# Optimization experiments

Measured on AMD Instinct MI355X. Metric: run time of the kernel, lower is better.

The kernel has to match this reference:

```python
import jax, jax.numpy as jnp
import numpy as np

B, N, I, H = 1024, 16, 256, 1024
V = 0.08  # init_var


def setup_inputs() -> dict:
    key = jax.random.key(0)
    ks = jax.random.split(key, 16)
    inp = jax.random.normal(ks[0], (B, N, I), jnp.float32)
    p = (jax.random.uniform(ks[1], (B, N, N)) > 0.3).astype(jnp.float32)
    phis = jnp.maximum(p, jnp.eye(N, dtype=jnp.float32)[None])  # ensure >=1 valid slot per row
    u = lambda k, s: jax.random.uniform(k, s, jnp.float32, -V, V)
    return {
        'input': inp, 'phis': phis,
        'init_token': jnp.zeros((I,), jnp.float32),
        'W1': u(ks[2], (H, H)), 'W2': u(ks[3], (H, H)), 'v': u(ks[4], (H, 1)),
        'Wih_e': u(ks[5], (3 * H, I)), 'Whh_e': u(ks[6], (3 * H, H)),
        'bih_e': u(ks[7], (3 * H,)), 'bhh_e': u(ks[8], (3 * H,)),
        'Wih_d': u(ks[9], (3 * H, I)), 'Whh_d': u(ks[10], (3 * H, H)),
        'bih_d': u(ks[11], (3 * H,)), 'bhh_d': u(ks[12], (3 * H,)),
    }


def gru_cell(x, h, Wih, Whh, bih, bhh):
    # torch.nn.GRUCell semantics; gate order [r, z, n]
    gi = x @ Wih.T + bih
    gh = h @ Whh.T + bhh
    ir, iz, ig = jnp.split(gi, 3, -1)
    hr, hz, hg = jnp.split(gh, 3, -1)
    r = jax.nn.sigmoid(ir + hr)
    z = jax.nn.sigmoid(iz + hz)
    g = jnp.tanh(ig + r * hg)
    return (1 - z) * g + z * h


def masked_softmax(mask, u):
    # faithful to softmax_m: mask before max, mask exps, normalize
    um = u * mask
    m = jnp.max(um, 1, keepdims=True)
    e = jnp.exp(um - m) * mask
    return e / jnp.sum(e, 1, keepdims=True)


def reference(input, phis, init_token, W1, W2, v,
              Wih_e, Whh_e, bih_e, bhh_e, Wih_d, Whh_d, bih_d, bhh_d):
    # gating scalar t_n = phis[:, n, n-1]; t_0 := 1 (no-op at step 0)
    t_gate = jnp.concatenate(
        [jnp.ones((B, 1), input.dtype), jnp.diagonal(phis, -1, 1, 2)], axis=1).T  # (N, B)

    # ---- Encoder ----
    def enc_step(h, xs):
        x, t = xs
        h = gru_cell(x, t[:, None] * h, Wih_e, Whh_e, bih_e, bhh_e)
        return h, h

    _, henc = jax.lax.scan(enc_step, jnp.zeros((B, H), input.dtype),
                           (input.transpose(1, 0, 2), t_gate))
    hidden_encoder = henc.transpose(1, 0, 2)  # (B, N, H)

    # ---- Decoder ----
    Ns = phis.sum(2)                                             # (B, N)
    idx_seq = ((Ns + jnp.arange(N)[None] - 1) % N).astype(jnp.int32)  # (B, N)
    bidx = jnp.arange(B)
    hidden0 = hidden_encoder[bidx, ((Ns[:, 0] - 1) % N).astype(jnp.int32)]  # (B, H)
    W1xe = jnp.einsum('bnh,hk->bnk', hidden_encoder, W1)         # (B, N, H)
    start = jnp.broadcast_to(init_token, (B, I))

    def dec_step(carry, xs):
        hidden, inp_step = carry
        t, idx, mask = xs
        init_h = hidden_encoder[bidx, idx]
        hidden = t[:, None] * hidden + (1 - t)[:, None] * init_h
        inp_step = t[:, None] * inp_step + (1 - t)[:, None] * start
        hidden = gru_cell(inp_step, hidden, Wih_d, Whh_d, bih_d, bhh_d)
        u = jnp.squeeze(jnp.tanh(W1xe + (hidden @ W2)[:, None, :]) @ v, -1)  # (B, N)
        attn = masked_softmax(mask, u)
        inp_step = jnp.einsum('bn,bni->bi', attn, input)
        return (hidden, inp_step), attn

    _, attns = jax.lax.scan(dec_step, (hidden0, start),
                            (t_gate, idx_seq.T, phis.transpose(1, 0, 2)))
    return attns.transpose(1, 0, 2)  # (B, N, N)
```

## Files before the change

kernel.cpp:

```cpp
#include <hip/hip_runtime.h>
#include <math.h>

#define B_  1024
#define N_  16
#define I_  256
#define H_  1024
#define H3_ 3072

typedef _Float16 f16;
typedef _Float16 f16x4 __attribute__((ext_vector_type(4)));
typedef _Float16 f16x8 __attribute__((ext_vector_type(8)));
typedef float    f32x4 __attribute__((ext_vector_type(4)));

__device__ __forceinline__ float sigmoidf_(float x) { return 1.f / (1.f + expf(-x)); }

__device__ __forceinline__ void lds_write_row(f16* dst, int row, int s, f16x8 vv)
{
    int key = (row >> 1) & 3;
    int g0  = (((s & 1) * 2 + 0) ^ key);
    int g1  = (((s & 1) * 2 + 1) ^ key);
    f16x4 lo = {vv[0], vv[1], vv[2], vv[3]};
    f16x4 hi = {vv[4], vv[5], vv[6], vv[7]};
    *(f16x4*)((char*)dst + row * 64 + g0 * 16 + (s >> 1) * 8) = lo;
    *(f16x4*)((char*)dst + row * 64 + g1 * 16 + (s >> 1) * 8) = hi;
}

__global__ void precompute_kernel(const float* __restrict__ phis,
                                  float* __restrict__ tg,
                                  int* __restrict__ idx)
{
    int b = blockIdx.x * blockDim.x + threadIdx.x;
    if (b >= B_) return;
    tg[b] = 1.0f;
    for (int t = 1; t < N_; ++t)
        tg[t * B_ + b] = phis[(size_t)b * N_ * N_ + t * N_ + (t - 1)];
    tg[16 * B_ + b] = 0.0f;
    for (int t = 0; t < N_; ++t) {
        float ns = 0.f;
        for (int k = 0; k < N_; ++k) ns += phis[(size_t)b * N_ * N_ + t * N_ + k];
        int nsi = (int)(ns + 0.5f);
        idx[b * N_ + t] = (nsi + t - 1) % N_;
    }
}

__global__ void cast_kernel(const float* __restrict__ in, f16* __restrict__ out, int n)
{
    int i = blockIdx.x * blockDim.x + threadIdx.x;
    if (i < n) out[i] = (f16)in[i];
}

__global__ void cast4_kernel(const float* __restrict__ s0, f16* __restrict__ d0, int n0,
                             const float* __restrict__ s1, f16* __restrict__ d1, int n1,
                             const float* __restrict__ s2, f16* __restrict__ d2, int n2,
                             const float* __restrict__ s3, f16* __restrict__ d3, int n3)
{
    int i = blockIdx.x * blockDim.x + threadIdx.x;
    int T0 = n0, T1 = T0 + n1, T2 = T1 + n2, T3 = T2 + n3;
    if (i < T0) d0[i] = (f16)s0[i];
    else if (i < T1) d1[i - T0] = (f16)s1[i - T0];
    else if (i < T2) d2[i - T1] = (f16)s2[i - T1];
    else if (i < T3) d3[i - T2] = (f16)s3[i - T2];
}

__global__ __launch_bounds__(256) void transpose_cast2_kernel(
    const float* __restrict__ in0, f16* __restrict__ out0,
    const float* __restrict__ in1, f16* __restrict__ out1)
{
    const float* in  = blockIdx.z ? in1 : in0;
    f16*        outp = blockIdx.z ? out1 : out0;
    __shared__ float tile[32][33];
    int bx = blockIdx.x * 32, by = blockIdx.y * 32;
    int tx = threadIdx.x & 31, ty = threadIdx.x >> 5;
#pragma unroll
    for (int r = 0; r < 32; r += 8)
        tile[ty + r][tx] = in[(size_t)(by + ty + r) * H_ + bx + tx];
    __syncthreads();
#pragma unroll
    for (int r = 0; r < 32; r += 8)
        outp[(size_t)(bx + ty + r) * H_ + by + tx] = (f16)tile[tx][ty + r];
}

template <typename OutT>
__global__ __launch_bounds__(256) void hgemm_kernel(
    const f16* __restrict__ A, int lda,
    const f16* __restrict__ Bt, int ldb,
    OutT* __restrict__ C, int ldc, int K)
{
    __shared__ char smem[32768];

    const int tid  = threadIdx.x;
    const int lane = tid & 63;
    const int wid  = tid >> 6;
    const int wr   = wid >> 1;
    const int wc   = wid & 1;
    const int rsel = lane & 15;
    const int kb   = lane >> 4;

    int flat = blockIdx.y * gridDim.x + blockIdx.x;
    int nwg  = gridDim.x * gridDim.y;
    int cpx  = nwg >> 3;
    int nf   = (flat & 7) * cpx + (flat >> 3);
    const int n0 = (int)(nf % gridDim.x) * 128;
    const int m0 = (int)(nf / gridDim.x) * 128;

    const int strow0 = tid >> 2;
    const int strow1 = 64 + (tid >> 2);
    const int sts    = tid & 3;

    f32x4 acc[4][4];
#pragma unroll
    for (int m = 0; m < 4; ++m)
#pragma unroll
        for (int n = 0; n < 4; ++n) acc[m][n] = (f32x4)0.f;

    f16x8 sA0, sA1, sB0, sB1;
    f16x8 tA0, tA1, tB0, tB1;
    auto GL0 = [&](int k0) {
        sA0 = *(const f16x8*)(A + (size_t)(m0 + strow0) * lda + k0 + sts * 8);
        sA1 = *(const f16x8*)(A + (size_t)(m0 + strow1) * lda + k0 + sts * 8);
        sB0 = *(const f16x8*)(Bt + (size_t)(n0 + strow0) * ldb + k0 + sts * 8);
        sB1 = *(const f16x8*)(Bt + (size_t)(n0 + strow1) * ldb + k0 + sts * 8);
    };
    auto GL1 = [&](int k0) {
        tA0 = *(const f16x8*)(A + (size_t)(m0 + strow0) * lda + k0 + sts * 8);
        tA1 = *(const f16x8*)(A + (size_t)(m0 + strow1) * lda + k0 + sts * 8);
        tB0 = *(const f16x8*)(Bt + (size_t)(n0 + strow0) * ldb + k0 + sts * 8);
        tB1 = *(const f16x8*)(Bt + (size_t)(n0 + strow1) * ldb + k0 + sts * 8);
    };
    auto LW0 = [&](int c) {
        f16* As_ = (f16*)(smem + c * 8192);
        f16* Bs_ = (f16*)(smem + 16384 + c * 8192);
        lds_write_row(As_, strow0, sts, sA0);
        lds_write_row(As_, strow1, sts, sA1);
        lds_write_row(Bs_, strow0, sts, sB0);
        lds_write_row(Bs_, strow1, sts, sB1);
    };
    auto LW1 = [&](int c) {
        f16* As_ = (f16*)(smem + c * 8192);
        f16* Bs_ = (f16*)(smem + 16384 + c * 8192);
        lds_write_row(As_, strow0, sts, tA0);
        lds_write_row(As_, strow1, sts, tA1);
        lds_write_row(Bs_, strow0, sts, tB0);
        lds_write_row(Bs_, strow1, sts, tB1);
    };
    auto COMP = [&](int c) {
        char* As_ = smem + c * 8192;
        char* Bs_ = smem + 16384 + c * 8192;
        f16x8 af[4], bf[4];
#pragma unroll
        for (int m = 0; m < 4; ++m) {
            int row = wr * 64 + m * 16 + rsel;
            af[m] = *(const f16x8*)(As_ + row * 64 + ((kb ^ ((row >> 1) & 3)) << 4));
        }
#pragma unroll
        for (int n = 0; n < 4; ++n) {
            int row = wc * 64 + n * 16 + rsel;
            bf[n] = *(const f16x8*)(Bs_ + row * 64 + ((kb ^ ((row >> 1) & 3)) << 4));
        }
#pragma unroll
        for (int m = 0; m < 4; ++m)
#pragma unroll
            for (int n = 0; n < 4; ++n)
                acc[m][n] = __builtin_amdgcn_mfma_f32_16x16x32_f16(af[m], bf[n], acc[m][n], 0, 0, 0);
    };

    const int nk = K / 32;
    GL0(0);
    GL1(32);
    LW0(0);
    __syncthreads();

    for (int ks = 0; ks < nk; ks += 2) {
        if (ks + 2 < nk) GL0((ks + 2) * 32);
        COMP(0);
        LW1(1);
        __syncthreads();
        if (ks + 3 < nk) GL1((ks + 3) * 32);
        COMP(1);
        if (ks + 2 < nk) LW0(0);
        __syncthreads();
    }

#pragma unroll
    for (int m = 0; m < 4; ++m) {
        int row0 = m0 + wr * 64 + m * 16 + kb * 4;
#pragma unroll
        for (int n = 0; n < 4; ++n) {
            int col = n0 + wc * 64 + n * 16 + rsel;
#pragma unroll
            for (int r = 0; r < 4; ++r)
                C[(size_t)(row0 + r) * ldc + col] = (OutT)acc[m][n][r];
        }
    }
}

template <int MODE>
__global__ __launch_bounds__(512) void gru_fused_kernel(
    const f16* __restrict__ A1, int lda1,
    const f16* __restrict__ Bt1, int ldb1, int K1,
    const f16* __restrict__ A2,
    const f16* __restrict__ Bt2,
    const float* __restrict__ bih, const float* __restrict__ bhh,
    float* __restrict__ h,
    const float* __restrict__ tg_cur,
    const float* __restrict__ tg_next,
    f16* __restrict__ out_a,
    f16* __restrict__ hs)
{
    __shared__ char smem[57344];

    const int tid  = threadIdx.x;
    const int wg   = tid >> 8;
    const int ltid = tid & 255;
    const int lane = tid & 63;
    const int wid4 = (ltid >> 6);
    const int wr   = wid4 >> 1;
    const int wc   = wid4 & 1;
    const int rsel = lane & 15;
    const int kb   = lane >> 4;

    char* base = smem + wg * 28672;

    int flat = blockIdx.y * gridDim.x + blockIdx.x;
    int nf   = (flat & 7) * 64 + (flat >> 3);
    const int j0 = (nf >> 5) * 64;
    const int b0 = (nf & 31) * 32;

    const int strow = ltid >> 2;
    const int sts   = ltid & 3;

    f32x4 acc1[3][2], acc2[3][2];
#pragma unroll
    for (int g = 0; g < 3; ++g)
#pragma unroll
        for (int nt = 0; nt < 2; ++nt) { acc1[g][nt] = (f32x4)0.f; acc2[g][nt] = (f32x4)0.f; }

    f16x8 sA, sB0, sB1, sB2;
    f16x8 tA, tB0, tB1, tB2;
    const f16* Ap;  const f16* Btp;  int ldap, ldbp;
    auto GL0 = [&](int k0) {
        if (ltid < 128) sA = *(const f16x8*)(Ap + (size_t)(b0 + strow) * ldap + k0 + sts * 8);
        sB0 = *(const f16x8*)(Btp + (size_t)(0 * H_ + j0 + strow) * ldbp + k0 + sts * 8);
        sB1 = *(const f16x8*)(Btp + (size_t)(1 * H_ + j0 + strow) * ldbp + k0 + sts * 8);
        sB2 = *(const f16x8*)(Btp + (size_t)(2 * H_ + j0 + strow) * ldbp + k0 + sts * 8);
    };
    auto GL1 = [&](int k0) {
        if (ltid < 128) tA = *(const f16x8*)(Ap + (size_t)(b0 + strow) * ldap + k0 + sts * 8);
        tB0 = *(const f16x8*)(Btp + (size_t)(0 * H_ + j0 + strow) * ldbp + k0 + sts * 8);
        tB1 = *(const f16x8*)(Btp + (size_t)(1 * H_ + j0 + strow) * ldbp + k0 + sts * 8);
        tB2 = *(const f16x8*)(Btp + (size_t)(2 * H_ + j0 + strow) * ldbp + k0 + sts * 8);
    };
    auto LW0 = [&](int c) {
        if (ltid < 128) lds_write_row((f16*)(base + c * 2048), strow, sts, sA);
        f16* Bs_ = (f16*)(base + 4096 + c * 12288);
        lds_write_row(Bs_ + 0 * 64 * 32, strow, sts, sB0);
        lds_write_row(Bs_ + 1 * 64 * 32, strow, sts, sB1);
        lds_write_row(Bs_ + 2 * 64 * 32, strow, sts, sB2);
    };
    auto LW1 = [&](int c) {
        if (ltid < 128) lds_write_row((f16*)(base + c * 2048), strow, sts, tA);
        f16* Bs_ = (f16*)(base + 4096 + c * 12288);
        lds_write_row(Bs_ + 0 * 64 * 32, strow, sts, tB0);
        lds_write_row(Bs_ + 1 * 64 * 32, strow, sts, tB1);
        lds_write_row(Bs_ + 2 * 64 * 32, strow, sts, tB2);
    };
    auto COMP = [&](int c, int phase) {
        char* As_ = base + c * 2048;
        char* Bs_ = base + 4096 + c * 12288;
        int arow = wr * 16 + rsel;
        f16x8 af = *(const f16x8*)(As_ + arow * 64 + ((kb ^ ((arow >> 1) & 3)) << 4));
#pragma unroll
        for (int gg = 0; gg < 3; ++gg)
#pragma unroll
            for (int nt = 0; nt < 2; ++nt) {
                int brow = wc * 32 + nt * 16 + rsel;
                f16x8 bf = *(const f16x8*)(Bs_ + (gg * 64 + brow) * 64 +
                                           ((kb ^ ((brow >> 1) & 3)) << 4));
                if (phase == 0)
                    acc1[gg][nt] = __builtin_amdgcn_mfma_f32_16x16x32_f16(af, bf, acc1[gg][nt], 0, 0, 0);
                else
                    acc2[gg][nt] = __builtin_amdgcn_mfma_f32_16x16x32_f16(af, bf, acc2[gg][nt], 0, 0, 0);
            }
    };

#pragma unroll
    for (int phase = 0; phase < 2; ++phase) {
        Ap   = phase ? A2 : A1;
        Btp  = phase ? Bt2 : Bt1;
        ldap = phase ? H_ : lda1;
        ldbp = phase ? H_ : ldb1;
        const int Kp   = phase ? H_ : K1;
        const int half = Kp >> 1;
        const int kbeg = wg * half;
        const int nk   = half >> 5;

        GL0(kbeg);
        GL1(kbeg + 32);
        LW0(0);
        __syncthreads();

        for (int ks = 0; ks < nk; ks += 2) {
            if (ks + 2 < nk) GL0(kbeg + (ks + 2) * 32);
            COMP(0, phase);
            LW1(1);
            __syncthreads();
            if (ks + 3 < nk) GL1(kbeg + (ks + 3) * 32);
            COMP(1, phase);
            if (ks + 2 < nk) LW0(0);
            __syncthreads();
        }
    }

    f32x4* red = (f32x4*)smem;
    if (wg) {
#pragma unroll
        for (int g = 0; g < 3; ++g)
#pragma unroll
            for (int nt = 0; nt < 2; ++nt) red[ltid * 6 + g * 2 + nt] = acc1[g][nt];
    }
    __syncthreads();
    if (!wg) {
#pragma unroll
        for (int g = 0; g < 3; ++g)
#pragma unroll
            for (int nt = 0; nt < 2; ++nt) acc1[g][nt] += red[ltid * 6 + g * 2 + nt];
    }
    __syncthreads();
    if (wg) {
#pragma unroll
        for (int g = 0; g < 3; ++g)
#pragma unroll
            for (int nt = 0; nt < 2; ++nt) red[ltid * 6 + g * 2 + nt] = acc2[g][nt];
    }
    __syncthreads();

    if (!wg) {
#pragma unroll
        for (int g = 0; g < 3; ++g)
#pragma unroll
            for (int nt = 0; nt < 2; ++nt) acc2[g][nt] += red[ltid * 6 + g * 2 + nt];

#pragma unroll
        for (int nt = 0; nt < 2; ++nt) {
            int j = j0 + wc * 32 + nt * 16 + rsel;
            float br_i = bih[j],          br_h = bhh[j];
            float bz_i = bih[H_ + j],     bz_h = bhh[H_ + j];
            float bg_i = bih[2 * H_ + j], bg_h = bhh[2 * H_ + j];
#pragma unroll
            for (int q = 0; q < 4; ++q) {
                int row = b0 + wr * 16 + kb * 4 + q;
                float r = sigmoidf_(acc1[0][nt][q] + br_i + acc2[0][nt][q] + br_h);
                float z = sigmoidf_(acc1[1][nt][q] + bz_i + acc2[1][nt][q] + bz_h);
                float g = tanhf(acc1[2][nt][q] + bg_i + r * (acc2[2][nt][q] + bg_h));
                float leak;
                if (MODE == 0) leak = tg_cur[row] * h[(size_t)row * H_ + j];
                else           leak = h[(size_t)row * H_ + j];
                float hn = (1.f - z) * g + z * leak;
                h[(size_t)row * H_ + j] = hn;
                if (MODE == 0) {
                    out_a[(size_t)row * (N_ * H_) + j] = (f16)hn;
                    hs[(size_t)row * H_ + j] = (f16)(tg_next[row] * hn);
                } else {
                    out_a[(size_t)row * H_ + j] = (f16)hn;
                }
            }
        }
    }
}

__global__ __launch_bounds__(512) void hgemm64_kernel(
    const f16* __restrict__ A, const f16* __restrict__ Bt, float* __restrict__ C)
{
    __shared__ char smem[32768];

    const int tid  = threadIdx.x;
    const int wg   = tid >> 8;
    const int ltid = tid & 255;
    const int lane = tid & 63;
    const int wid4 = (ltid >> 6);
    const int wr   = wid4 >> 1;
    const int wc   = wid4 & 1;
    const int rsel = lane & 15;
    const int kb   = lane >> 4;

    char* base = smem + wg * 16384;

    int flat = blockIdx.y * gridDim.x + blockIdx.x;
    int nf   = (flat & 7) * 32 + (flat >> 3);
    const int m0 = (nf >> 4) * 64;
    const int n0 = (nf & 15) * 64;

    const int strow = ltid >> 2;
    const int sts   = ltid & 3;

    f32x4 acc[2][2];
#pragma unroll
    for (int m = 0; m < 2; ++m)
#pragma unroll
        for (int n = 0; n < 2; ++n) acc[m][n] = (f32x4)0.f;

    f16x8 sA, sB, tA, tB;
    auto GL0 = [&](int k0) {
        sA = *(const f16x8*)(A + (size_t)(m0 + strow) * H_ + k0 + sts * 8);
        sB = *(const f16x8*)(Bt + (size_t)(n0 + strow) * H_ + k0 + sts * 8);
    };
    auto GL1 = [&](int k0) {
        tA = *(const f16x8*)(A + (size_t)(m0 + strow) * H_ + k0 + sts * 8);
        tB = *(const f16x8*)(Bt + (size_t)(n0 + strow) * H_ + k0 + sts * 8);
    };
    auto LW0 = [&](int c) {
        lds_write_row((f16*)(base + c * 4096), strow, sts, sA);
        lds_write_row((f16*)(base + 8192 + c * 4096), strow, sts, sB);
    };
    auto LW1 = [&](int c) {
        lds_write_row((f16*)(base + c * 4096), strow, sts, tA);
        lds_write_row((f16*)(base + 8192 + c * 4096), strow, sts, tB);
    };
    auto COMP = [&](int c) {
        char* As_ = base + c * 4096;
        char* Bs_ = base + 8192 + c * 4096;
        f16x8 af[2], bf[2];
#pragma unroll
        for (int m = 0; m < 2; ++m) {
            int row = wr * 32 + m * 16 + rsel;
            af[m] = *(const f16x8*)(As_ + row * 64 + ((kb ^ ((row >> 1) & 3)) << 4));
        }
#pragma unroll
        for (int nt = 0; nt < 2; ++nt) {
            int row = wc * 32 + nt * 16 + rsel;
            bf[nt] = *(const f16x8*)(Bs_ + row * 64 + ((kb ^ ((row >> 1) & 3)) << 4));
        }
#pragma unroll
        for (int m = 0; m < 2; ++m)
#pragma unroll
            for (int nt = 0; nt < 2; ++nt)
                acc[m][nt] = __builtin_amdgcn_mfma_f32_16x16x32_f16(af[m], bf[nt], acc[m][nt], 0, 0, 0);
    };

    const int kbeg = wg * 512;
    GL0(kbeg);
    GL1(kbeg + 32);
    LW0(0);
    __syncthreads();

    for (int ks = 0; ks < 16; ks += 2) {
        if (ks + 2 < 16) GL0(kbeg + (ks + 2) * 32);
        COMP(0);
        LW1(1);
        __syncthreads();
        if (ks + 3 < 16) GL1(kbeg + (ks + 3) * 32);
        COMP(1);
        if (ks + 2 < 16) LW0(0);
        __syncthreads();
    }

    f32x4* red = (f32x4*)smem;
    if (wg) {
#pragma unroll
        for (int m = 0; m < 2; ++m)
#pragma unroll
            for (int nt = 0; nt < 2; ++nt) red[ltid * 4 + m * 2 + nt] = acc[m][nt];
    }
    __syncthreads();
    if (!wg) {
#pragma unroll
        for (int m = 0; m < 2; ++m)
#pragma unroll
            for (int nt = 0; nt < 2; ++nt) {
                acc[m][nt] += red[ltid * 4 + m * 2 + nt];
                int col = n0 + wc * 32 + nt * 16 + rsel;
#pragma unroll
                for (int q = 0; q < 4; ++q) {
                    int row = m0 + wr * 32 + m * 16 + kb * 4 + q;
                    C[(size_t)row * H_ + col] = acc[m][nt][q];
                }
            }
    }
}

__global__ void dec_init_kernel(float* __restrict__ h, f16* __restrict__ hs,
                                const f16* __restrict__ he, const int* __restrict__ idx)
{
    int i = blockIdx.x * blockDim.x + threadIdx.x;
    int b = i >> 10;
    int j = i & (H_ - 1);
    float v0 = (float)he[(size_t)b * N_ * H_ + (size_t)idx[b * N_] * H_ + j];
    h[i]  = v0;
    hs[i] = (f16)v0;
}

__global__ void init_input_kernel(f16* __restrict__ inp, const float* __restrict__ tok)
{
    int i = blockIdx.x * blockDim.x + threadIdx.x;
    inp[i] = (f16)tok[i & (I_ - 1)];
}

template <int MIX>
__global__ __launch_bounds__(1024) void attn_kernel(
    const f16*   __restrict__ w1xe,
    const float* __restrict__ hw2,
    const float* __restrict__ v,
    const float* __restrict__ phis,
    const f16*   __restrict__ in16,
    float* __restrict__ out,
    f16*   __restrict__ inp_step,
    int t,
    const float* __restrict__ tg_next,
    const int*   __restrict__ idx_next,
    const f16*   __restrict__ he,
    float* __restrict__ h,
    f16*   __restrict__ hs,
    const float* __restrict__ tok)
{
    int b   = blockIdx.x;
    int tid = threadIdx.x;
    int w   = tid >> 6;
    int l   = tid & 63;
    __shared__ float un[N_];
    __shared__ float attns[N_];

    {
        const f16*   wrow = w1xe + ((size_t)(b * N_ + w)) * H_;
        const float* hwp  = hw2 + (size_t)b * H_;
        f16x8 w0 = *(const f16x8*)(wrow + l * 8);
        f16x8 w1 = *(const f16x8*)(wrow + 512 + l * 8);
        f32x4 h0 = *(const f32x4*)(hwp + l * 8);
        f32x4 h1 = *(const f32x4*)(hwp + l * 8 + 4);
        f32x4 h2 = *(const f32x4*)(hwp + 512 + l * 8);
        f32x4 h3 = *(const f32x4*)(hwp + 512 + l * 8 + 4);
        f32x4 v0 = *(const f32x4*)(v + l * 8);
        f32x4 v1 = *(const f32x4*)(v + l * 8 + 4);
        f32x4 v2 = *(const f32x4*)(v + 512 + l * 8);
        f32x4 v3 = *(const f32x4*)(v + 512 + l * 8 + 4);
        float s = 0.f;
#pragma unroll
        for (int e = 0; e < 4; ++e) {
            s += tanhf((float)w0[e]     + h0[e]) * v0[e];
            s += tanhf((float)w0[e + 4] + h1[e]) * v1[e];
            s += tanhf((float)w1[e]     + h2[e]) * v2[e];
            s += tanhf((float)w1[e + 4] + h3[e]) * v3[e];
        }
#pragma unroll
        for (int off = 32; off; off >>= 1) s += __shfl_down(s, off, 64);
        if (l == 0) un[w] = s;
    }
    __syncthreads();

    if (tid < N_) {
        float mk = phis[(size_t)b * N_ * N_ + t * N_ + tid];
        float um = un[tid] * mk;
        float m = um;
#pragma unroll
        for (int off = 1; off < 16; off <<= 1) m = fmaxf(m, __shfl_xor(m, off, 16));
        float e = expf(um - m) * mk;
        float ssum = e;
#pragma unroll
        for (int off = 1; off < 16; off <<= 1) ssum += __shfl_xor(ssum, off, 16);
        float a = e / ssum;
        attns[tid] = a;
        out[(size_t)b * N_ * N_ + t * N_ + tid] = a;
    }
    __syncthreads();

    if (tid < I_) {
        float acc = 0.f;
#pragma unroll
        for (int n = 0; n < N_; ++n)
            acc += attns[n] * (float)in16[((size_t)b * N_ + n) * I_ + tid];
        if (MIX) {
            float tn = tg_next[b];
            inp_step[(size_t)b * I_ + tid] = (f16)(tn * acc + (1.f - tn) * tok[tid]);
        } else {
            inp_step[(size_t)b * I_ + tid] = (f16)acc;
        }
    }

    if (MIX) {
        float tn = tg_next[b];
        int id = idx_next[b * N_];
        float ih = (float)he[(size_t)b * N_ * H_ + (size_t)id * H_ + tid];
        float hm = tn * h[(size_t)b * H_ + tid] + (1.f - tn) * ih;
        h[(size_t)b * H_ + tid]  = hm;
        hs[(size_t)b * H_ + tid] = (f16)hm;
    }
}

extern "C" void kernel_launch(void* const* d_in, const int* in_sizes, int n_in,
                              void* d_out, int out_size, void* d_ws, size_t ws_size,
                              hipStream_t stream)
{
    const float* input      = (const float*)d_in[0];
    const float* phis       = (const float*)d_in[1];
    const float* init_token = (const float*)d_in[2];
    const float* W1         = (const float*)d_in[3];
    const float* W2         = (const float*)d_in[4];
    const float* v          = (const float*)d_in[5];
    const float* Wih_e      = (const float*)d_in[6];
    const float* Whh_e      = (const float*)d_in[7];
    const float* bih_e      = (const float*)d_in[8];
    const float* bhh_e      = (const float*)d_in[9];
    const float* Wih_d      = (const float*)d_in[10];
    const float* Whh_d      = (const float*)d_in[11];
    const float* bih_d      = (const float*)d_in[12];
    const float* bhh_d      = (const float*)d_in[13];
    float* out = (float*)d_out;

    char* p = (char*)d_ws;
    f16*  he16    = (f16*)p;  p += (size_t)B_ * N_ * H_ * 2;
    f16*  w1xe16  = (f16*)p;  p += (size_t)B_ * N_ * H_ * 2;
    float* h      = (float*)p; p += (size_t)B_ * H_ * 4;
    f16*  hs16    = (f16*)p;  p += (size_t)2 * B_ * H_ * 2;
    f16*  hc16    = (f16*)p;  p += (size_t)B_ * H_ * 2;
    f16*  inp16   = (f16*)p;  p += (size_t)B_ * I_ * 2;
    float* hw2    = (float*)p; p += (size_t)B_ * H_ * 4;
    f16*  in16    = (f16*)p;  p += (size_t)B_ * N_ * I_ * 2;
    f16*  Wih_e16 = (f16*)p;  p += (size_t)H3_ * I_ * 2;
    f16*  Whh_e16 = (f16*)p;  p += (size_t)H3_ * H_ * 2;
    f16*  Wih_d16 = (f16*)p;  p += (size_t)H3_ * I_ * 2;
    f16*  Whh_d16 = (f16*)p;  p += (size_t)H3_ * H_ * 2;
    f16*  W1t16   = (f16*)p;  p += (size_t)H_ * H_ * 2;
    f16*  W2t16   = (f16*)p;  p += (size_t)H_ * H_ * 2;
    float* tg     = (float*)p; p += (size_t)17 * B_ * 4;
    int*   idx    = (int*)p;   p += (size_t)B_ * N_ * 4;

    const size_t BH = (size_t)B_ * H_;
    const int BHBLK = (B_ * H_) / 256;
    const int BIBLK = (B_ * I_) / 256;
    const dim3 gru_grid(16, 32);

    precompute_kernel<<<4, 256, 0, stream>>>(phis, tg, idx);

    cast_kernel<<<(B_ * N_ * I_) / 256, 256, 0, stream>>>(input, in16, B_ * N_ * I_);
    cast4_kernel<<<(2 * (H3_ * I_ + H3_ * H_)) / 256, 256, 0, stream>>>(
        Wih_e, Wih_e16, H3_ * I_, Whh_e, Whh_e16, H3_ * H_,
        Wih_d, Wih_d16, H3_ * I_, Whh_d, Whh_d16, H3_ * H_);
    transpose_cast2_kernel<<<dim3(32, 32, 2), 256, 0, stream>>>(W1, W1t16, W2, W2t16);

    hipMemsetAsync(h, 0, BH * 4, stream);
    hipMemsetAsync(hs16, 0, BH * 2, stream);
    for (int t = 0; t < N_; ++t) {
        gru_fused_kernel<0><<<gru_grid, 512, 0, stream>>>(
            in16 + (size_t)t * I_, N_ * I_, Wih_e16, I_, I_,
            hs16 + (size_t)(t & 1) * BH, Whh_e16, bih_e, bhh_e, h,
            tg + (size_t)t * B_, tg + (size_t)(t + 1) * B_,
            he16 + (size_t)t * H_, hs16 + (size_t)((t + 1) & 1) * BH);
    }

    hgemm_kernel<f16><<<dim3(H_ / 128, (B_ * N_) / 128), 256, 0, stream>>>(
        he16, H_, W1t16, H_, w1xe16, H_, H_);

    dec_init_kernel<<<BHBLK, 256, 0, stream>>>(h, hs16, he16, idx);
    init_input_kernel<<<BIBLK, 256, 0, stream>>>(inp16, init_token);
    for (int t = 0; t < N_; ++t) {
        gru_fused_kernel<1><<<gru_grid, 512, 0, stream>>>(
            inp16, I_, Wih_d16, I_, I_,
            hs16, Whh_d16, bih_d, bhh_d, h,
            nullptr, nullptr, hc16, nullptr);
        hgemm64_kernel<<<dim3(16, 16), 512, 0, stream>>>(hc16, W2t16, hw2);
        if (t < N_ - 1)
            attn_kernel<1><<<B_, 1024, 0, stream>>>(
                w1xe16, hw2, v, phis, in16, out, inp16, t,
                tg + (size_t)(t + 1) * B_, idx + (t + 1), he16, h, hs16, init_token);
        else
            attn_kernel<0><<<B_, 1024, 0, stream>>>(
                w1xe16, hw2, v, phis, in16, out, inp16, t,
                tg, idx, he16, h, hs16, init_token);
    }
}
```

Measured before the change: 1.282 ms.

## Merge GRU GEMM phases into one pipeline, quadruple split-K in hgemm64, fuse init

The fused GRU kernel's two GEMM phases (input-hidden and hidden-hidden) now run as one continuous double-buffered K loop. This removes the pipeline drain and refill, plus a barrier, at the phase boundary. The 64x64 hgemm kernel grows from 2 to 4 split-K warpgroups (1024 threads, 64KB LDS) to get more parallelism on the small per-step W2 GEMM, with a 3-way LDS reduction at the end. The init_input kernel is folded into dec_init to save one launch. The extra LDS and threads may reduce occupancy, and the longer reduction adds some overhead.

```diff
diff --git a/kernel.cpp b/kernel.cpp
--- a/kernel.cpp
+++ b/kernel.cpp
@@ -229,6 +229,9 @@
     const int strow = ltid >> 2;
     const int sts   = ltid & 3;
 
+    const int nk0 = (K1 >> 1) >> 5;
+    const int NT  = nk0 + ((H_ >> 1) >> 5);
+
     f32x4 acc1[3][2], acc2[3][2];
 #pragma unroll
     for (int g = 0; g < 3; ++g)
@@ -237,18 +240,26 @@
 
     f16x8 sA, sB0, sB1, sB2;
     f16x8 tA, tB0, tB1, tB2;
-    const f16* Ap;  const f16* Btp;  int ldap, ldbp;
-    auto GL0 = [&](int k0) {
-        if (ltid < 128) sA = *(const f16x8*)(Ap + (size_t)(b0 + strow) * ldap + k0 + sts * 8);
-        sB0 = *(const f16x8*)(Btp + (size_t)(0 * H_ + j0 + strow) * ldbp + k0 + sts * 8);
-        sB1 = *(const f16x8*)(Btp + (size_t)(1 * H_ + j0 + strow) * ldbp + k0 + sts * 8);
-        sB2 = *(const f16x8*)(Btp + (size_t)(2 * H_ + j0 + strow) * ldbp + k0 + sts * 8);
-    };
-    auto GL1 = [&](int k0) {
-        if (ltid < 128) tA = *(const f16x8*)(Ap + (size_t)(b0 + strow) * ldap + k0 + sts * 8);
-        tB0 = *(const f16x8*)(Btp + (size_t)(0 * H_ + j0 + strow) * ldbp + k0 + sts * 8);
-        tB1 = *(const f16x8*)(Btp + (size_t)(1 * H_ + j0 + strow) * ldbp + k0 + sts * 8);
-        tB2 = *(const f16x8*)(Btp + (size_t)(2 * H_ + j0 + strow) * ldbp + k0 + sts * 8);
+
+    auto srcAddr = [&](int i, const f16*& Aq, const f16*& Bq, int& la, int& lb, int& k0) {
+        if (i < nk0) { Aq = A1; Bq = Bt1; la = lda1; lb = ldb1; k0 = wg * (K1 >> 1) + i * 32; }
+        else         { Aq = A2; Bq = Bt2; la = H_;   lb = H_;   k0 = wg * (H_ >> 1) + (i - nk0) * 32; }
+    };
+    auto GL0 = [&](int i) {
+        const f16 *Aq, *Bq; int la, lb, k0;
+        srcAddr(i, Aq, Bq, la, lb, k0);
+        if (ltid < 128) sA = *(const f16x8*)(Aq + (size_t)(b0 + strow) * la + k0 + sts * 8);
+        sB0 = *(const f16x8*)(Bq + (size_t)(0 * H_ + j0 + strow) * lb + k0 + sts * 8);
+        sB1 = *(const f16x8*)(Bq + (size_t)(1 * H_ + j0 + strow) * lb + k0 + sts * 8);
+        sB2 = *(const f16x8*)(Bq + (size_t)(2 * H_ + j0 + strow) * lb + k0 + sts * 8);
+    };
+    auto GL1 = [&](int i) {
+        const f16 *Aq, *Bq; int la, lb, k0;
+        srcAddr(i, Aq, Bq, la, lb, k0);
+        if (ltid < 128) tA = *(const f16x8*)(Aq + (size_t)(b0 + strow) * la + k0 + sts * 8);
+        tB0 = *(const f16x8*)(Bq + (size_t)(0 * H_ + j0 + strow) * lb + k0 + sts * 8);
+        tB1 = *(const f16x8*)(Bq + (size_t)(1 * H_ + j0 + strow) * lb + k0 + sts * 8);
+        tB2 = *(const f16x8*)(Bq + (size_t)(2 * H_ + j0 + strow) * lb + k0 + sts * 8);
     };
     auto LW0 = [&](int c) {
         if (ltid < 128) lds_write_row((f16*)(base + c * 2048), strow, sts, sA);
@@ -264,51 +275,48 @@
         lds_write_row(Bs_ + 1 * 64 * 32, strow, sts, tB1);
         lds_write_row(Bs_ + 2 * 64 * 32, strow, sts, tB2);
     };
-    auto COMP = [&](int c, int phase) {
+    auto COMP = [&](int c, int ph) {
         char* As_ = base + c * 2048;
         char* Bs_ = base + 4096 + c * 12288;
         int arow = wr * 16 + rsel;
         f16x8 af = *(const f16x8*)(As_ + arow * 64 + ((kb ^ ((arow >> 1) & 3)) << 4));
-#pragma unroll
-        for (int gg = 0; gg < 3; ++gg)
-#pragma unroll
-            for (int nt = 0; nt < 2; ++nt) {
-                int brow = wc * 32 + nt * 16 + rsel;
-                f16x8 bf = *(const f16x8*)(Bs_ + (gg * 64 + brow) * 64 +
-                                           ((kb ^ ((brow >> 1) & 3)) << 4));
-                if (phase == 0)
+        if (ph == 0) {
+#pragma unroll
+            for (int gg = 0; gg < 3; ++gg)
+#pragma unroll
+                for (int nt = 0; nt < 2; ++nt) {
+                    int brow = wc * 32 + nt * 16 + rsel;
+                    f16x8 bf = *(const f16x8*)(Bs_ + (gg * 64 + brow) * 64 +
+                                               ((kb ^ ((brow >> 1) & 3)) << 4));
                     acc1[gg][nt] = __builtin_amdgcn_mfma_f32_16x16x32_f16(af, bf, acc1[gg][nt], 0, 0, 0);
-                else
+                }
+        } else {
+#pragma unroll
+            for (int gg = 0; gg < 3; ++gg)
+#pragma unroll
+                for (int nt = 0; nt < 2; ++nt) {
+                    int brow = wc * 32 + nt * 16 + rsel;
+                    f16x8 bf = *(const f16x8*)(Bs_ + (gg * 64 + brow) * 64 +
+                                               ((kb ^ ((brow >> 1) & 3)) << 4));
                     acc2[gg][nt] = __builtin_amdgcn_mfma_f32_16x16x32_f16(af, bf, acc2[gg][nt], 0, 0, 0);
-            }
-    };
-
-#pragma unroll
-    for (int phase = 0; phase < 2; ++phase) {
-        Ap   = phase ? A2 : A1;
-        Btp  = phase ? Bt2 : Bt1;
-        ldap = phase ? H_ : lda1;
-        ldbp = phase ? H_ : ldb1;
-        const int Kp   = phase ? H_ : K1;
-        const int half = Kp >> 1;
-        const int kbeg = wg * half;
-        const int nk   = half >> 5;
-
-        GL0(kbeg);
-        GL1(kbeg + 32);
-        LW0(0);
+                }
+        }
+    };
+
+    GL0(0);
+    GL1(1);
+    LW0(0);
+    __syncthreads();
+
+    for (int i = 0; i < NT; i += 2) {
+        if (i + 2 < NT) GL0(i + 2);
+        COMP(0, (i < nk0) ? 0 : 1);
+        LW1(1);
         __syncthreads();
-
-        for (int ks = 0; ks < nk; ks += 2) {
-            if (ks + 2 < nk) GL0(kbeg + (ks + 2) * 32);
-            COMP(0, phase);
-            LW1(1);
-            __syncthreads();
-            if (ks + 3 < nk) GL1(kbeg + (ks + 3) * 32);
-            COMP(1, phase);
-            if (ks + 2 < nk) LW0(0);
-            __syncthreads();
-        }
+        if (i + 3 < NT) GL1(i + 3);
+        COMP(1, ((i + 1) < nk0) ? 0 : 1);
+        if (i + 2 < NT) LW0(0);
+        __syncthreads();
     }
 
     f32x4* red = (f32x4*)smem;
@@ -368,10 +376,10 @@
     }
 }
 
-__global__ __launch_bounds__(512) void hgemm64_kernel(
+__global__ __launch_bounds__(1024) void hgemm64_kernel(
     const f16* __restrict__ A, const f16* __restrict__ Bt, float* __restrict__ C)
 {
-    __shared__ char smem[32768];
+    __shared__ char smem[65536];
 
     const int tid  = threadIdx.x;
     const int wg   = tid >> 8;
@@ -437,20 +445,20 @@
                 acc[m][nt] = __builtin_amdgcn_mfma_f32_16x16x32_f16(af[m], bf[nt], acc[m][nt], 0, 0, 0);
     };
 
-    const int kbeg = wg * 512;
+    const int kbeg = wg * 256;
     GL0(kbeg);
     GL1(kbeg + 32);
     LW0(0);
     __syncthreads();
 
-    for (int ks = 0; ks < 16; ks += 2) {
-        if (ks + 2 < 16) GL0(kbeg + (ks + 2) * 32);
+    for (int ks = 0; ks < 8; ks += 2) {
+        if (ks + 2 < 8) GL0(kbeg + (ks + 2) * 32);
         COMP(0);
         LW1(1);
         __syncthreads();
-        if (ks + 3 < 16) GL1(kbeg + (ks + 3) * 32);
+        if (ks + 3 < 8) GL1(kbeg + (ks + 3) * 32);
         COMP(1);
-        if (ks + 2 < 16) LW0(0);
+        if (ks + 2 < 8) LW0(0);
         __syncthreads();
     }
 
@@ -459,7 +467,8 @@
 #pragma unroll
         for (int m = 0; m < 2; ++m)
 #pragma unroll
-            for (int nt = 0; nt < 2; ++nt) red[ltid * 4 + m * 2 + nt] = acc[m][nt];
+            for (int nt = 0; nt < 2; ++nt)
+                red[((size_t)(wg - 1) * 256 + ltid) * 4 + m * 2 + nt] = acc[m][nt];
     }
     __syncthreads();
     if (!wg) {
@@ -467,7 +476,9 @@
         for (int m = 0; m < 2; ++m)
 #pragma unroll
             for (int nt = 0; nt < 2; ++nt) {
-                acc[m][nt] += red[ltid * 4 + m * 2 + nt];
+#pragma unroll
+                for (int w = 0; w < 3; ++w)
+                    acc[m][nt] += red[((size_t)w * 256 + ltid) * 4 + m * 2 + nt];
                 int col = n0 + wc * 32 + nt * 16 + rsel;
 #pragma unroll
                 for (int q = 0; q < 4; ++q) {
@@ -479,7 +490,8 @@
 }
 
 __global__ void dec_init_kernel(float* __restrict__ h, f16* __restrict__ hs,
-                                const f16* __restrict__ he, const int* __restrict__ idx)
+                                const f16* __restrict__ he, const int* __restrict__ idx,
+                                f16* __restrict__ inp, const float* __restrict__ tok)
 {
     int i = blockIdx.x * blockDim.x + threadIdx.x;
     int b = i >> 10;
@@ -487,12 +499,7 @@
     float v0 = (float)he[(size_t)b * N_ * H_ + (size_t)idx[b * N_] * H_ + j];
     h[i]  = v0;
     hs[i] = (f16)v0;
-}
-
-__global__ void init_input_kernel(f16* __restrict__ inp, const float* __restrict__ tok)
-{
-    int i = blockIdx.x * blockDim.x + threadIdx.x;
-    inp[i] = (f16)tok[i & (I_ - 1)];
+    if (i < B_ * I_) inp[i] = (f16)tok[i & (I_ - 1)];
 }
 
 template <int MIX>
@@ -625,7 +632,6 @@
 
     const size_t BH = (size_t)B_ * H_;
     const int BHBLK = (B_ * H_) / 256;
-    const int BIBLK = (B_ * I_) / 256;
     const dim3 gru_grid(16, 32);
 
     precompute_kernel<<<4, 256, 0, stream>>>(phis, tg, idx);
@@ -649,14 +655,13 @@
     hgemm_kernel<f16><<<dim3(H_ / 128, (B_ * N_) / 128), 256, 0, stream>>>(
         he16, H_, W1t16, H_, w1xe16, H_, H_);
 
-    dec_init_kernel<<<BHBLK, 256, 0, stream>>>(h, hs16, he16, idx);
-    init_input_kernel<<<BIBLK, 256, 0, stream>>>(inp16, init_token);
+    dec_init_kernel<<<BHBLK, 256, 0, stream>>>(h, hs16, he16, idx, inp16, init_token);
     for (int t = 0; t < N_; ++t) {
         gru_fused_kernel<1><<<gru_grid, 512, 0, stream>>>(
             inp16, I_, Wih_d16, I_, I_,
             hs16, Whh_d16, bih_d, bhh_d, h,
             nullptr, nullptr, hc16, nullptr);
-        hgemm64_kernel<<<dim3(16, 16), 512, 0, stream>>>(hc16, W2t16, hw2);
+        hgemm64_kernel<<<dim3(16, 16), 1024, 0, stream>>>(hc16, W2t16, hw2);
         if (t < N_ - 1)
             attn_kernel<1><<<B_, 1024, 0, stream>>>(
                 w1xe16, hw2, v, phis, in16, out, inp16, t,
```

Measured after the change: 1.905 ms. +48.6%, slower.
